# Kernel optimization log

Measured on AMD Instinct MI355X. Metric: run time of the kernel, lower is better.

## Reference

```python
import jax, jax.numpy as jnp
import numpy as np
from jax import lax

B, C_IN, H_IN, W_IN = 128, 256, 8, 32
RH, RW = 16, 64            # rec-head resolution
YOH, XOH = RH // 2, RW // 2  # onehot sizes (8, 32)
HID = 256
NC = 163                   # num classes == embed size
T = 32                     # target length
C_ENC = C_IN + XOH + YOH   # 296 encoder channels
L = (RH // 2) * (RW // 2)  # 256 attention positions


def setup_inputs() -> dict:
    key = jax.random.key(0)
    ks = jax.random.split(key, 18)
    s = 0.05
    return {
        "x": jax.random.normal(ks[0], (B, C_IN, H_IN, W_IN), jnp.float32),
        "decoder_targets": jax.random.randint(ks[1], (B, T), 0, NC),
        "word_targets": jax.random.randint(ks[2], (B, T), 0, NC),
        # seq_encoder conv 3x3
        "conv_w": jax.random.normal(ks[3], (C_IN, C_IN, 3, 3), jnp.float32) * 0.02,
        "conv_b": jnp.zeros((C_IN,), jnp.float32),
        # decoder embedding (post kaiming re-init => random, not identity)
        "emb_dec": jax.random.normal(ks[4], (NC, NC), jnp.float32) * s,
        "word_w": jax.random.normal(ks[5], (HID, NC), jnp.float32) * s,
        "word_b": jnp.zeros((HID,), jnp.float32),
        "attn_w": jax.random.normal(ks[6], (HID, 2 * HID + XOH + YOH), jnp.float32) * s,
        "attn_b": jnp.zeros((HID,), jnp.float32),
        "attn_v": jax.random.normal(ks[7], (HID,), jnp.float32) * (1.0 / np.sqrt(HID)),
        # GRUCell, gate order [r, z, n]
        "gru_wih": jax.random.normal(ks[8], (3 * HID, 2 * HID + XOH + YOH), jnp.float32) * s,
        "gru_bih": jnp.zeros((3 * HID,), jnp.float32),
        "gru_whh": jax.random.normal(ks[9], (3 * HID, HID), jnp.float32) * s,
        "gru_bhh": jnp.zeros((3 * HID,), jnp.float32),
        "out_w": jax.random.normal(ks[10], (NC, HID), jnp.float32) * s,
        "out_b": jnp.zeros((NC,), jnp.float32),
        # positional one-hot embedding tables (also kaiming re-initialized)
        "x_emb": jax.random.normal(ks[11], (XOH, XOH), jnp.float32) * s,
        "y_emb": jax.random.normal(ks[12], (YOH, YOH), jnp.float32) * s,
    }


def _forward(x, conv_w, conv_b, emb_dec, word_w, word_b, attn_w, attn_b, attn_v,
             gru_wih, gru_bih, gru_whh, gru_bhh, out_w, out_b, x_emb, y_emb,
             decoder_targets, word_targets):
    b = x.shape[0]
    # rescale: bilinear upsample (align_corners=False ~ half-pixel)
    xr = jax.image.resize(x, (b, C_IN, RH, RW), method="linear")
    # seq_encoder: conv3x3 + ReLU + maxpool2
    conv = lax.conv_general_dilated(xr, conv_w, (1, 1), "SAME",
                                    dimension_numbers=("NCHW", "OIHW", "NCHW"))
    conv = jax.nn.relu(conv + conv_b[None, :, None, None])
    pooled = lax.reduce_window(conv, -jnp.inf, lax.max,
                               (1, 1, 2, 2), (1, 1, 2, 2), "VALID")  # (B,256,8,32)
    hf, wf = RH // 2, RW // 2
    # positional channels: x_map[c,y,x] = x_emb[x,c]; y_map[c,y,x] = y_emb[y,c]
    x_map = jnp.broadcast_to(x_emb.T[:, None, :], (XOH, hf, wf))
    y_map = jnp.broadcast_to(y_emb.T[:, :, None], (YOH, hf, wf))
    x_map = jnp.broadcast_to(x_map[None], (b, XOH, hf, wf))
    y_map = jnp.broadcast_to(y_map[None], (b, YOH, hf, wf))
    feat = jnp.concatenate([pooled, x_map, y_map], axis=1)      # (B,296,8,32)
    enc = feat.reshape(b, C_ENC, hf * wf).transpose(0, 2, 1)    # (B, L, C)

    t_len = decoder_targets.shape[1]
    # teacher forcing: input at step 0 is BOS (=0), else previous target
    inputs_seq = jnp.concatenate(
        [jnp.zeros((b, 1), decoder_targets.dtype), decoder_targets[:, :-1]], axis=1)

    def step(hidden, xs):
        tok, tgt = xs
        we = emb_dec[tok] @ word_w.T + word_b                   # (B, HID)
        # Bahdanau attention
        hrep = jnp.broadcast_to(hidden[:, None, :], (b, enc.shape[1], HID))
        cat = jnp.concatenate([hrep, enc], axis=-1)             # (B,L,2H+OH)
        energy = jnp.tanh(jnp.einsum("blc,hc->blh", cat, attn_w) + attn_b)
        scores = jnp.einsum("blh,h->bl", energy, attn_v)
        w = jax.nn.softmax(scores, axis=1)                      # (B,L)
        ctx = jnp.einsum("bl,blc->bc", w, enc)                  # (B, C)
        rin = jnp.concatenate([we, ctx], axis=-1)               # (B, 2H+OH)
        # GRUCell
        gi = rin @ gru_wih.T + gru_bih
        gh = hidden @ gru_whh.T + gru_bhh
        i_r, i_z, i_n = jnp.split(gi, 3, axis=-1)
        h_r, h_z, h_n = jnp.split(gh, 3, axis=-1)
        r = jax.nn.sigmoid(i_r + h_r)
        z = jax.nn.sigmoid(i_z + h_z)
        n = jnp.tanh(i_n + r * h_n)
        h_new = (1.0 - z) * n + z * hidden
        logp = jax.nn.log_softmax(h_new @ out_w.T + out_b, axis=1)
        # NLLLoss(ignore_index=-1, reduction='none')
        nll = -jnp.take_along_axis(logp, jnp.clip(tgt, 0)[:, None], axis=1)[:, 0]
        nll = jnp.where(tgt >= 0, nll, 0.0)
        return h_new, nll

    h0 = jnp.zeros((b, HID), jnp.float32)
    _, nlls = lax.scan(step, h0, (inputs_seq.T, word_targets.T))  # (T, B)
    loss_vec = nlls.sum(axis=0)                                   # (B,)
    return 0.2 * (loss_vec.sum() / loss_vec.shape[0])


def reference(x, decoder_targets, word_targets, conv_w, conv_b, emb_dec,
              word_w, word_b, attn_w, attn_b, attn_v, gru_wih, gru_bih,
              gru_whh, gru_bhh, out_w, out_b, x_emb, y_emb):
    return _forward(x, conv_w, conv_b, emb_dec, word_w, word_b, attn_w, attn_b,
                    attn_v, gru_wih, gru_bih, gru_whh, gru_bhh, out_w, out_b,
                    x_emb, y_emb, decoder_targets, word_targets)
```

## Files before the change

### kernel.cpp

```cpp
#include <hip/hip_runtime.h>
#include <hip/hip_bf16.h>
#include <math.h>

#define B    128
#define CIN  256
#define HIN  8
#define WIN_ 32
#define RH   16
#define RW   64
#define HID  256
#define NC   163
#define T    32
#define L    256
#define CENC 296

typedef __attribute__((ext_vector_type(8))) short short8;
typedef __attribute__((ext_vector_type(8))) unsigned short u16x8;
typedef __attribute__((ext_vector_type(4))) float f32x4;

__device__ __forceinline__ float bf2f(unsigned short u) {
    unsigned int x = ((unsigned int)u) << 16;
    return __uint_as_float(x);
}
__device__ __forceinline__ unsigned short f2bf(float f) {
    unsigned int x = __float_as_uint(f);
    unsigned int r = (x + 0x7FFFu + ((x >> 16) & 1u)) >> 16;
    return (unsigned short)r;
}
__device__ __forceinline__ float fast_tanh(float x) {
    float e = __expf(2.f * x);
    return 1.f - 2.f * __builtin_amdgcn_rcpf(e + 1.f);
}
__device__ __forceinline__ float fast_sigm(float x) {
    return __builtin_amdgcn_rcpf(1.f + __expf(-x));
}
__device__ __forceinline__ float wave_red_max(float v) {
    #pragma unroll
    for (int o = 32; o > 0; o >>= 1) v = fmaxf(v, __shfl_down(v, o, 64));
    return v;
}
__device__ __forceinline__ float wave_red_sum(float v) {
    #pragma unroll
    for (int o = 32; o > 0; o >>= 1) v += __shfl_down(v, o, 64);
    return v;
}
__device__ __forceinline__ float half_red_sum(float v) {
    #pragma unroll
    for (int o = 16; o > 0; o >>= 1) v += __shfl_down(v, o, 64);
    return v;
}

__global__ void __launch_bounds__(256) k_upsxt(const float* __restrict__ x,
                                               unsigned short* __restrict__ Xt) {
    __shared__ __align__(16) float sf[64 * 2 * 32];
    const int y = blockIdx.x;
    const int b = blockIdx.y;
    const int tid = threadIdx.x;
    float sy = 0.5f * y - 0.25f;
    int yq0 = (y - 1) >> 1;
    float wy = sy - (float)yq0;
    int y0c = min(max(yq0, 0), HIN - 1);
    int y1c = min(max(yq0 + 1, 0), HIN - 1);
    const int xo = tid & 63;
    const int cj = tid >> 6;
    float sx = 0.5f * xo - 0.25f;
    int xq0 = (xo - 1) >> 1;
    float wx = sx - (float)xq0;
    int x0c = min(max(xq0, 0), WIN_ - 1);
    int x1c = min(max(xq0 + 1, 0), WIN_ - 1);
    for (int cc = 0; cc < 4; cc++) {
        __syncthreads();
        #pragma unroll
        for (int i = 0; i < 4; i++) {
            int idx = tid * 4 + i;
            int c = idx >> 4;
            int rowh = (idx >> 3) & 1;
            int part = idx & 7;
            int ysrc = rowh ? y1c : y0c;
            float4 v = *reinterpret_cast<const float4*>(
                x + ((size_t)(b * CIN + cc * 64 + c) * HIN + ysrc) * WIN_ + part * 4);
            *reinterpret_cast<float4*>(sf + ((c * 2 + rowh) * 32 + part * 4)) = v;
        }
        __syncthreads();
        unsigned short ov[16];
        #pragma unroll
        for (int j = 0; j < 16; j++) {
            int c = cj * 16 + j;
            const float* r0 = sf + (c * 2 + 0) * 32;
            const float* r1 = sf + (c * 2 + 1) * 32;
            float v = (1.f - wy) * ((1.f - wx) * r0[x0c] + wx * r0[x1c])
                    +        wy  * ((1.f - wx) * r1[x0c] + wx * r1[x1c]);
            ov[j] = f2bf(v);
        }
        unsigned short* dst = Xt + ((size_t)((b * 16 + y) * 64 + xo)) * 256 + cc * 64 + cj * 16;
        *reinterpret_cast<u16x8*>(dst)     = *reinterpret_cast<u16x8*>(ov);
        *reinterpret_cast<u16x8*>(dst + 8) = *reinterpret_cast<u16x8*>(ov + 8);
    }
}

__global__ void k_wt(const float* __restrict__ conv_w, unsigned short* __restrict__ Wt) {
    int e = blockIdx.x * 256 + threadIdx.x;
    int ci = e & 255;
    int co = (e >> 8) & 255;
    int s  = e >> 16;
    Wt[(size_t)(s * 256 + co) * 256 + ci] = f2bf(conv_w[(size_t)(co * 256 + ci) * 9 + s]);
}

__global__ void __launch_bounds__(256) k_convmm(const unsigned short* __restrict__ Xt,
        const unsigned short* __restrict__ Wt, const float* __restrict__ conv_b,
        unsigned short* __restrict__ enc_bf) {
    __shared__ __align__(16) char smem[36864];
    unsigned short* A_s = (unsigned short*)smem;
    unsigned short* B_s = A_s + 128 * 72;
    float* pool = (float*)smem;
    const int mt = blockIdx.x;
    const int n0 = blockIdx.y * 128;
    const int b = mt >> 3;
    const int y0 = (mt & 7) * 2;
    const int tid = threadIdx.x;
    const int wave = tid >> 6, lane = tid & 63;
    const int mq = (wave & 1) * 64, nq = (wave >> 1) * 64;
    const int lm = lane & 15, lq = lane >> 4;
    f32x4 acc[4][4];
    #pragma unroll
    for (int mi = 0; mi < 4; mi++)
        #pragma unroll
        for (int ni = 0; ni < 4; ni++)
            #pragma unroll
            for (int r = 0; r < 4; r++) acc[mi][ni][r] = 0.f;

    for (int s9 = 0; s9 < 9; s9++) {
        const int ky = s9 / 3, kx = s9 % 3;
        const unsigned short* Wb = Wt + (size_t)s9 * 256 * 256;
        for (int kc = 0; kc < 256; kc += 64) {
            __syncthreads();
            #pragma unroll
            for (int it = 0; it < 8; it++) {
                int s2 = tid + it * 256;
                int i = s2 & 1023;
                int row = i >> 3, q8 = i & 7;
                if (s2 < 1024) {
                    int yy = y0 + (row >> 6) + ky - 1;
                    int xx = (row & 63) + kx - 1;
                    u16x8 va = {0, 0, 0, 0, 0, 0, 0, 0};
                    if ((unsigned)yy < 16u && (unsigned)xx < 64u)
                        va = *reinterpret_cast<const u16x8*>(
                            Xt + ((size_t)((b * 16 + yy) * 64 + xx)) * 256 + kc + q8 * 8);
                    *reinterpret_cast<u16x8*>(A_s + row * 72 + q8 * 8) = va;
                } else {
                    u16x8 vb = *reinterpret_cast<const u16x8*>(
                        Wb + (size_t)(n0 + row) * 256 + kc + q8 * 8);
                    *reinterpret_cast<u16x8*>(B_s + row * 72 + q8 * 8) = vb;
                }
            }
            __syncthreads();
            for (int ks = 0; ks < 2; ks++) {
                short8 af[4], bfr[4];
                #pragma unroll
                for (int mi = 0; mi < 4; mi++)
                    af[mi] = *reinterpret_cast<const short8*>(
                        A_s + (mq + mi * 16 + lm) * 72 + ks * 32 + lq * 8);
                #pragma unroll
                for (int ni = 0; ni < 4; ni++)
                    bfr[ni] = *reinterpret_cast<const short8*>(
                        B_s + (nq + ni * 16 + lm) * 72 + ks * 32 + lq * 8);
                #pragma unroll
                for (int mi = 0; mi < 4; mi++)
                    #pragma unroll
                    for (int ni = 0; ni < 4; ni++)
                        acc[mi][ni] = __builtin_amdgcn_mfma_f32_16x16x32_bf16(
                            af[mi], bfr[ni], acc[mi][ni], 0, 0, 0);
            }
        }
    }
    __syncthreads();
    #pragma unroll
    for (int mi = 0; mi < 4; mi++) {
        int px0 = mi * 8 + lq * 2;
        #pragma unroll
        for (int ni = 0; ni < 4; ni++) {
            int nl = nq + ni * 16 + lm;
            float pa = fmaxf(acc[mi][ni][0], acc[mi][ni][1]);
            float pb = fmaxf(acc[mi][ni][2], acc[mi][ni][3]);
            pool[((wave & 1) * 32 + px0) * 132 + nl] = pa;
            pool[((wave & 1) * 32 + px0 + 1) * 132 + nl] = pb;
        }
    }
    __syncthreads();
    {
        int base = tid * 16;
        int px = base >> 7;
        int nb = base & 127;
        unsigned short ov[16];
        #pragma unroll
        for (int i = 0; i < 16; i++) {
            int n = nb + i;
            float v = fmaxf(pool[px * 132 + n], pool[(32 + px) * 132 + n]) + conv_b[n0 + n];
            ov[i] = f2bf(fmaxf(v, 0.f));
        }
        unsigned short* dst = enc_bf + ((size_t)b * L + (mt & 7) * 32 + px) * CENC + n0 + nb;
        *reinterpret_cast<u16x8*>(dst)     = *reinterpret_cast<u16x8*>(ov);
        *reinterpret_cast<u16x8*>(dst + 8) = *reinterpret_cast<u16x8*>(ov + 8);
    }
}

__global__ void k_encpos(const float* __restrict__ x_emb, const float* __restrict__ y_emb,
                         unsigned short* __restrict__ enc_bf, unsigned short* __restrict__ pos2t) {
    int b = blockIdx.x, l = threadIdx.x;
    int yl = l >> 5, xl = l & 31;
    unsigned short* e = enc_bf + (size_t)(b * L + l) * CENC + 256;
    #pragma unroll
    for (int c = 0; c < 32; c++) e[c] = f2bf(x_emb[xl * 32 + c]);
    #pragma unroll
    for (int c = 0; c < 8; c++) e[32 + c] = f2bf(y_emb[yl * 8 + c]);
    if (b == 0) {
        #pragma unroll
        for (int c = 0; c < 32; c++) pos2t[c * 256 + l] = f2bf(x_emb[xl * 32 + c]);
        #pragma unroll
        for (int c = 0; c < 8; c++) pos2t[(32 + c) * 256 + l] = f2bf(y_emb[yl * 8 + c]);
    }
}

__global__ void __launch_bounds__(256) k_enct(const unsigned short* __restrict__ enc_bf,
                                              unsigned short* __restrict__ enc_t) {
    __shared__ unsigned short s[64 * 264];
    const int c0 = blockIdx.x * 64;
    const int b = blockIdx.y;
    const int tid = threadIdx.x;
    #pragma unroll
    for (int j = 0; j < 8; j++) {
        u16x8 u = *reinterpret_cast<const u16x8*>(
            enc_bf + ((size_t)b * L + tid) * CENC + c0 + j * 8);
        #pragma unroll
        for (int k = 0; k < 8; k++) s[(j * 8 + k) * 264 + tid] = u[k];
    }
    __syncthreads();
    {
        int c = tid >> 2, lp = tid & 3;
        const unsigned short* row = s + c * 264 + lp * 64;
        unsigned short* dst = enc_t + ((size_t)b * 256 + c0 + c) * L + lp * 64;
        #pragma unroll
        for (int i = 0; i < 8; i++)
            *reinterpret_cast<u16x8*>(dst + i * 8) =
                *reinterpret_cast<const u16x8*>(row + i * 8);
    }
}

__global__ void __launch_bounds__(256) k_etab(const float* __restrict__ emb_dec,
                                              const float* __restrict__ word_w,
                                              const float* __restrict__ word_b,
                                              float* __restrict__ E) {
    __shared__ float er[NC];
    int row = blockIdx.x, tid = threadIdx.x;
    for (int k = tid; k < NC; k += 256) er[k] = emb_dec[(size_t)row * NC + k];
    __syncthreads();
    float a = word_b[tid];
    for (int k = 0; k < NC; k++) a += er[k] * word_w[(size_t)tid * NC + k];
    E[(size_t)row * HID + tid] = a;
}

__global__ void k_prep(const float* __restrict__ attn_w, const float* __restrict__ out_w,
                       unsigned short* __restrict__ wA_bf, unsigned short* __restrict__ ow_bf) {
    int o = blockIdx.x, k = threadIdx.x;
    wA_bf[(size_t)o * 256 + k] = f2bf(attn_w[(size_t)o * 552 + k]);
    if (o < NC) ow_bf[(size_t)o * 256 + k] = f2bf(out_w[(size_t)o * 256 + k]);
}

__global__ void __launch_bounds__(1024) k_wpack(const float* __restrict__ wih,
        const float* __restrict__ whh, unsigned short* __restrict__ WpackC,
        unsigned short* __restrict__ WpackH) {
    const int blk = blockIdx.x;
    const int tid = threadIdx.x;
    unsigned short o[8];
    if (blk < 37) {
        #pragma unroll
        for (int j = 0; j < 8; j++) {
            int k = blk * 8 + j;
            float v = (tid < 768) ? wih[(size_t)tid * 552 + 256 + k] : 0.f;
            o[j] = f2bf(v);
        }
        *reinterpret_cast<u16x8*>(WpackC + ((size_t)blk * 1024 + tid) * 8) =
            *reinterpret_cast<u16x8*>(o);
    } else {
        int it = blk - 37;
        #pragma unroll
        for (int j = 0; j < 8; j++) {
            int k = it * 8 + j;
            float v = (tid < 768) ? whh[(size_t)tid * 256 + k] : 0.f;
            o[j] = f2bf(v);
        }
        *reinterpret_cast<u16x8*>(WpackH + ((size_t)it * 1024 + tid) * 8) =
            *reinterpret_cast<u16x8*>(o);
    }
}

__global__ void __launch_bounds__(768) k_wge(const float* __restrict__ wih,
                                             unsigned short* __restrict__ WgE) {
    int k = blockIdx.x, g = threadIdx.x;
    WgE[(size_t)k * 768 + g] = f2bf(wih[(size_t)g * 552 + k]);
}
__global__ void __launch_bounds__(768) k_gie(const float* __restrict__ E,
                                             const unsigned short* __restrict__ WgE,
                                             const float* __restrict__ bih,
                                             float* __restrict__ giE) {
    __shared__ float er[256];
    int v = blockIdx.x, g = threadIdx.x;
    if (g < 256) er[g] = E[(size_t)v * 256 + g];
    __syncthreads();
    float a = bih[g];
    #pragma unroll 4
    for (int k = 0; k < 256; k++) a += er[k] * bf2f(WgE[(size_t)k * 768 + g]);
    giE[(size_t)v * 768 + g] = a;
}

__global__ void __launch_bounds__(256) k_ep(const unsigned short* __restrict__ enc_bf,
                                            const float* __restrict__ attn_w,
                                            unsigned short* __restrict__ ep_t) {
    __shared__ __align__(16) float eS[16][132];
    __shared__ __align__(16) float wS[16][36];
    const int l0 = blockIdx.x * 128;
    const int h0 = blockIdx.y * 32;
    const int b = blockIdx.z;
    const int tid = threadIdx.x;
    const int hh = tid >> 5, ll = tid & 31;
    float acc[4][4];
    #pragma unroll
    for (int s2 = 0; s2 < 4; s2++)
        #pragma unroll
        for (int r = 0; r < 4; r++) acc[s2][r] = 0.f;
    for (int kc = 0; kc < CENC; kc += 16) {
        const int kn = min(16, CENC - kc);
        __syncthreads();
        #pragma unroll
        for (int it = 0; it < 2; it++) {
            int idx = it * 256 + tid;
            int lq = idx >> 2, kq = idx & 3;
            float v0 = 0.f, v1 = 0.f, v2 = 0.f, v3 = 0.f;
            if (kq * 4 < kn) {
                ushort4 u = *reinterpret_cast<const ushort4*>(
                    enc_bf + (size_t)(b * L + l0 + lq) * CENC + kc + kq * 4);
                v0 = bf2f(u.x); v1 = bf2f(u.y); v2 = bf2f(u.z); v3 = bf2f(u.w);
            }
            eS[kq * 4 + 0][lq] = v0; eS[kq * 4 + 1][lq] = v1;
            eS[kq * 4 + 2][lq] = v2; eS[kq * 4 + 3][lq] = v3;
        }
        if (tid < 128) {
            int hq = tid >> 2, kq = tid & 3;
            float4 v = make_float4(0.f, 0.f, 0.f, 0.f);
            if (kq * 4 < kn)
                v = *reinterpret_cast<const float4*>(attn_w + (size_t)(h0 + hq) * 552 + 256 + kc + kq * 4);
            wS[kq * 4 + 0][hq] = v.x; wS[kq * 4 + 1][hq] = v.y;
            wS[kq * 4 + 2][hq] = v.z; wS[kq * 4 + 3][hq] = v.w;
        }
        __syncthreads();
        #pragma unroll
        for (int k = 0; k < 16; k++) {
            float4 e = *reinterpret_cast<const float4*>(&eS[k][ll * 4]);
            float4 w = *reinterpret_cast<const float4*>(&wS[k][hh * 4]);
            float ev[4] = {e.x, e.y, e.z, e.w};
            float wv[4] = {w.x, w.y, w.z, w.w};
            #pragma unroll
            for (int s2 = 0; s2 < 4; s2++)
                #pragma unroll
                for (int r = 0; r < 4; r++) acc[s2][r] += wv[s2] * ev[r];
        }
    }
    #pragma unroll
    for (int r = 0; r < 4; r++) {
        ushort4 o;
        o.x = f2bf(acc[0][r]); o.y = f2bf(acc[1][r]);
        o.z = f2bf(acc[2][r]); o.w = f2bf(acc[3][r]);
        *reinterpret_cast<ushort4*>(
            ep_t + ((size_t)(b * L) + l0 + ll * 4 + r) * HID + h0 + hh * 4) = o;
    }
}

__global__ void k_init(int* __restrict__ flagH, int* __restrict__ flagS) {
    if (threadIdx.x < B) { flagH[threadIdx.x] = 0; flagS[threadIdx.x] = 0; }
}

__global__ void __launch_bounds__(1024) k_steps(
        const float* __restrict__ giE, const float* __restrict__ bhh,
        const unsigned short* __restrict__ ep_t, const unsigned short* __restrict__ enc_t,
        const unsigned short* __restrict__ wA_bf, const unsigned short* __restrict__ ow_bf,
        const unsigned short* __restrict__ pos2t,
        const unsigned short* __restrict__ WpackC, const unsigned short* __restrict__ WpackH,
        const float* __restrict__ attn_b, const float* __restrict__ attn_v,
        const float* __restrict__ out_b,
        const int* __restrict__ dec_tgt, const int* __restrict__ word_tgt,
        float* __restrict__ nllG,
        unsigned int* __restrict__ hX32, unsigned int* __restrict__ sX32,
        int* __restrict__ flagH, int* __restrict__ flagS) {
    const int bid = blockIdx.x;
    const bool roleA = bid < B;
    const int b = bid & (B - 1);
    const int tid = threadIdx.x;
    const int hwid = tid >> 5, l32 = tid & 31;

    __shared__ __align__(16) unsigned short big[L * 256];
    __shared__ __align__(16) unsigned short hmail[256];
    __shared__ __align__(16) unsigned short swl[256];
    __shared__ __align__(16) float rinF[552];
    __shared__ __align__(16) float hF[256];
    __shared__ __align__(16) float hpF[256], vbF[256], swlF[256];
    __shared__ float hfS[256];
    __shared__ float scr[256];
    __shared__ float red[16];
    __shared__ float rzS[512], inS[256], hnS[256];
    unsigned int* hmail32 = reinterpret_cast<unsigned int*>(hmail);
    unsigned int* swl32 = reinterpret_cast<unsigned int*>(swl);

    if (roleA) {
        if (tid < 256) vbF[tid] = attn_v[tid];
        {
            const u16x8* src = reinterpret_cast<const u16x8*>(ep_t + (size_t)b * L * 256);
            u16x8* dst = reinterpret_cast<u16x8*>(big);
            #pragma unroll
            for (int i = 0; i < 8; i++) dst[tid + i * 1024] = src[tid + i * 1024];
        }
        float nllacc = 0.f;
        __syncthreads();
        for (int t = 0; t <= T; t++) {
            if (tid == 0) {
                while (__hip_atomic_load(&flagH[b], __ATOMIC_RELAXED,
                                         __HIP_MEMORY_SCOPE_AGENT) < t + 1)
                    __builtin_amdgcn_s_sleep(1);
            }
            __syncthreads();
            if (tid < 128) {
                unsigned int u = __hip_atomic_load(&hX32[b * 128 + tid], __ATOMIC_RELAXED,
                                                   __HIP_MEMORY_SCOPE_AGENT);
                hF[2 * tid]     = bf2f((unsigned short)(u & 0xffffu));
                hF[2 * tid + 1] = bf2f((unsigned short)(u >> 16));
            }
            __syncthreads();
            if (t < T) {
                #pragma unroll
                for (int it = 0; it < 8; it++) {
                    int row = it * 32 + hwid;
                    u16x8 w = *reinterpret_cast<const u16x8*>(wA_bf + (size_t)row * 256 + l32 * 8);
                    float4 ha = *reinterpret_cast<const float4*>(hF + l32 * 8);
                    float4 hb = *reinterpret_cast<const float4*>(hF + l32 * 8 + 4);
                    float d = bf2f(w[0]) * ha.x + bf2f(w[1]) * ha.y
                            + bf2f(w[2]) * ha.z + bf2f(w[3]) * ha.w
                            + bf2f(w[4]) * hb.x + bf2f(w[5]) * hb.y
                            + bf2f(w[6]) * hb.z + bf2f(w[7]) * hb.w;
                    d = half_red_sum(d);
                    if (l32 == 0) hpF[row] = d + attn_b[row];
                }
                __syncthreads();
                #pragma unroll
                for (int it = 0; it < 8; it++) {
                    int row = it * 32 + hwid;
                    u16x8 e = *reinterpret_cast<const u16x8*>(big + (size_t)row * 256 + l32 * 8);
                    float4 ha = *reinterpret_cast<const float4*>(hpF + l32 * 8);
                    float4 hb = *reinterpret_cast<const float4*>(hpF + l32 * 8 + 4);
                    float4 va = *reinterpret_cast<const float4*>(vbF + l32 * 8);
                    float4 vv = *reinterpret_cast<const float4*>(vbF + l32 * 8 + 4);
                    float d = va.x * fast_tanh(bf2f(e[0]) + ha.x)
                            + va.y * fast_tanh(bf2f(e[1]) + ha.y)
                            + va.z * fast_tanh(bf2f(e[2]) + ha.z)
                            + va.w * fast_tanh(bf2f(e[3]) + ha.w)
                            + vv.x * fast_tanh(bf2f(e[4]) + hb.x)
                            + vv.y * fast_tanh(bf2f(e[5]) + hb.y)
                            + vv.z * fast_tanh(bf2f(e[6]) + hb.z)
                            + vv.w * fast_tanh(bf2f(e[7]) + hb.w);
                    d = half_red_sum(d);
                    if (l32 == 0) scr[row] = d;
                }
                __syncthreads();
                float sc = -1e30f;
                if (tid < 256) {
                    sc = scr[tid];
                    float m = wave_red_max(sc);
                    if ((tid & 63) == 0) red[tid >> 6] = m;
                }
                __syncthreads();
                float M2 = fmaxf(fmaxf(red[0], red[1]), fmaxf(red[2], red[3]));
                float e2 = 0.f;
                if (tid < 256) {
                    e2 = __expf(sc - M2);
                    float sm = wave_red_sum(e2);
                    if ((tid & 63) == 0) red[8 + (tid >> 6)] = sm;
                }
                __syncthreads();
                if (tid < 256) {
                    float invS = __builtin_amdgcn_rcpf(red[8] + red[9] + red[10] + red[11]);
                    swl[tid] = f2bf(e2 * invS);
                }
                __syncthreads();
                if (tid < 128)
                    __hip_atomic_store(&sX32[b * 128 + tid], swl32[tid], __ATOMIC_RELAXED,
                                       __HIP_MEMORY_SCOPE_AGENT);
                __syncthreads();
                if (tid == 0)
                    __hip_atomic_store(&flagS[b], t + 1, __ATOMIC_RELAXED,
                                       __HIP_MEMORY_SCOPE_AGENT);
            }
            if (t > 0) {
                #pragma unroll
                for (int it = 0; it < 6; it++) {
                    int row = it * 32 + hwid;
                    float d = 0.f;
                    if (row < NC) {
                        u16x8 w = *reinterpret_cast<const u16x8*>(ow_bf + (size_t)row * 256 + l32 * 8);
                        float4 ha = *reinterpret_cast<const float4*>(hF + l32 * 8);
                        float4 hb = *reinterpret_cast<const float4*>(hF + l32 * 8 + 4);
                        d = bf2f(w[0]) * ha.x + bf2f(w[1]) * ha.y
                          + bf2f(w[2]) * ha.z + bf2f(w[3]) * ha.w
                          + bf2f(w[4]) * hb.x + bf2f(w[5]) * hb.y
                          + bf2f(w[6]) * hb.z + bf2f(w[7]) * hb.w;
                    }
                    d = half_red_sum(d);
                    if (l32 == 0 && row < NC) scr[row] = d + out_b[row];
                }
                __syncthreads();
                float lg = -1e30f;
                if (tid < 256) {
                    if (tid < NC) lg = scr[tid];
                    float m = wave_red_max(lg);
                    if ((tid & 63) == 0) red[tid >> 6] = m;
                }
                __syncthreads();
                float M = fmaxf(fmaxf(red[0], red[1]), fmaxf(red[2], red[3]));
                if (tid < 256) {
                    float e = (tid < NC) ? __expf(lg - M) : 0.f;
                    float sm = wave_red_sum(e);
                    if ((tid & 63) == 0) red[8 + (tid >> 6)] = sm;
                }
                __syncthreads();
                if (tid == 0) {
                    float S = red[8] + red[9] + red[10] + red[11];
                    int tgt = word_tgt[b * T + (t - 1)];
                    if (tgt >= 0) nllacc += M + __logf(S) - scr[tgt];
                }
                __syncthreads();
            }
        }
        if (tid == 0) nllG[b] = nllacc;
    } else {
        {
            const u16x8* src = reinterpret_cast<const u16x8*>(enc_t + (size_t)b * 256 * 256);
            u16x8* dst = reinterpret_cast<u16x8*>(big);
            #pragma unroll
            for (int i = 0; i < 8; i++) dst[tid + i * 1024] = src[tid + i * 1024];
        }
        __syncthreads();
        for (int t = 0; t <= T; t++) {
            if (tid < 256) {
                float h;
                if (t == 0) {
                    h = 0.f;
                } else {
                    float hold = hfS[tid];
                    int tokp = (t == 1) ? 0 : dec_tgt[b * T + (t - 2)];
                    const float* gE = giE + (size_t)tokp * 768;
                    float r_ = fast_sigm(rzS[tid] + gE[tid] + bhh[tid]);
                    float z_ = fast_sigm(rzS[256 + tid] + gE[256 + tid] + bhh[256 + tid]);
                    float n_ = fast_tanh(inS[tid] + gE[512 + tid] + r_ * (hnS[tid] + bhh[512 + tid]));
                    h = (1.f - z_) * n_ + z_ * hold;
                }
                hfS[tid] = h;
                hmail[tid] = f2bf(h);
                rinF[296 + tid] = h;
            }
            __syncthreads();
            if (tid < 128)
                __hip_atomic_store(&hX32[b * 128 + tid], hmail32[tid], __ATOMIC_RELAXED,
                                   __HIP_MEMORY_SCOPE_AGENT);
            __syncthreads();
            if (tid == 0)
                __hip_atomic_store(&flagH[b], t + 1, __ATOMIC_RELAXED,
                                   __HIP_MEMORY_SCOPE_AGENT);
            if (t == T) break;
            float hacc = 0.f;
            if (tid < 768) {
                float a0 = 0.f, a1 = 0.f;
                #pragma unroll 4
                for (int it = 0; it < 32; it++) {
                    u16x8 w = *reinterpret_cast<const u16x8*>(WpackH + ((size_t)it * 1024 + tid) * 8);
                    float4 ra = *reinterpret_cast<const float4*>(rinF + 296 + it * 8);
                    float4 rb = *reinterpret_cast<const float4*>(rinF + 296 + it * 8 + 4);
                    a0 += bf2f(w[0]) * ra.x + bf2f(w[2]) * ra.z
                        + bf2f(w[4]) * rb.x + bf2f(w[6]) * rb.z;
                    a1 += bf2f(w[1]) * ra.y + bf2f(w[3]) * ra.w
                        + bf2f(w[5]) * rb.y + bf2f(w[7]) * rb.w;
                }
                hacc = a0 + a1;
            }
            if (tid == 0) {
                while (__hip_atomic_load(&flagS[b], __ATOMIC_RELAXED,
                                         __HIP_MEMORY_SCOPE_AGENT) < t + 1)
                    __builtin_amdgcn_s_sleep(1);
            }
            __syncthreads();
            if (tid < 128) {
                unsigned int u = __hip_atomic_load(&sX32[b * 128 + tid], __ATOMIC_RELAXED,
                                                   __HIP_MEMORY_SCOPE_AGENT);
                swlF[2 * tid]     = bf2f((unsigned short)(u & 0xffffu));
                swlF[2 * tid + 1] = bf2f((unsigned short)(u >> 16));
            }
            __syncthreads();
            #pragma unroll
            for (int it = 0; it < 8; it++) {
                int row = it * 32 + hwid;
                u16x8 e = *reinterpret_cast<const u16x8*>(big + (size_t)row * 256 + l32 * 8);
                float4 sa = *reinterpret_cast<const float4*>(swlF + l32 * 8);
                float4 sb = *reinterpret_cast<const float4*>(swlF + l32 * 8 + 4);
                float d = bf2f(e[0]) * sa.x + bf2f(e[1]) * sa.y
                        + bf2f(e[2]) * sa.z + bf2f(e[3]) * sa.w
                        + bf2f(e[4]) * sb.x + bf2f(e[5]) * sb.y
                        + bf2f(e[6]) * sb.z + bf2f(e[7]) * sb.w;
                d = half_red_sum(d);
                if (l32 == 0) rinF[row] = d;
            }
            #pragma unroll
            for (int it = 0; it < 2; it++) {
                int row = it * 32 + hwid;
                float d = 0.f;
                if (row < 40) {
                    u16x8 p = *reinterpret_cast<const u16x8*>(pos2t + (size_t)row * 256 + l32 * 8);
                    float4 sa = *reinterpret_cast<const float4*>(swlF + l32 * 8);
                    float4 sb = *reinterpret_cast<const float4*>(swlF + l32 * 8 + 4);
                    d = bf2f(p[0]) * sa.x + bf2f(p[1]) * sa.y
                      + bf2f(p[2]) * sa.z + bf2f(p[3]) * sa.w
                      + bf2f(p[4]) * sb.x + bf2f(p[5]) * sb.y
                      + bf2f(p[6]) * sb.z + bf2f(p[7]) * sb.w;
                }
                d = half_red_sum(d);
                if (l32 == 0 && row < 40) rinF[256 + row] = d;
            }
            __syncthreads();
            if (tid < 768) {
                float c0 = 0.f, c1 = 0.f;
                #pragma unroll 4
                for (int it = 0; it < 37; it++) {
                    u16x8 w = *reinterpret_cast<const u16x8*>(WpackC + ((size_t)it * 1024 + tid) * 8);
                    float4 ra = *reinterpret_cast<const float4*>(rinF + it * 8);
                    float4 rb = *reinterpret_cast<const float4*>(rinF + it * 8 + 4);
                    c0 += bf2f(w[0]) * ra.x + bf2f(w[2]) * ra.z
                        + bf2f(w[4]) * rb.x + bf2f(w[6]) * rb.z;
                    c1 += bf2f(w[1]) * ra.y + bf2f(w[3]) * ra.w
                        + bf2f(w[5]) * rb.y + bf2f(w[7]) * rb.w;
                }
                float cacc = c0 + c1;
                if (tid < 512) rzS[tid] = cacc + hacc;
                else { inS[tid - 512] = cacc; hnS[tid - 512] = hacc; }
            }
            __syncthreads();
        }
    }
}

__global__ void k_reduce(const float* __restrict__ nll, float* __restrict__ out) {
    __shared__ float red[2];
    float v = nll[threadIdx.x];
    v = wave_red_sum(v);
    if ((threadIdx.x & 63) == 0) red[threadIdx.x >> 6] = v;
    __syncthreads();
    if (threadIdx.x == 0) out[0] = 0.2f * (red[0] + red[1]) * (1.f / 128.f);
}

extern "C" void kernel_launch(void* const* d_in, const int* in_sizes, int n_in,
                              void* d_out, int out_size, void* d_ws, size_t ws_size,
                              hipStream_t stream) {
    const float* x        = (const float*)d_in[0];
    const int*   dec_tgt  = (const int*)d_in[1];
    const int*   word_tgt = (const int*)d_in[2];
    const float* conv_w   = (const float*)d_in[3];
    const float* conv_b   = (const float*)d_in[4];
    const float* emb_dec  = (const float*)d_in[5];
    const float* word_w   = (const float*)d_in[6];
    const float* word_b   = (const float*)d_in[7];
    const float* attn_w   = (const float*)d_in[8];
    const float* attn_b   = (const float*)d_in[9];
    const float* attn_v   = (const float*)d_in[10];
    const float* gru_wih  = (const float*)d_in[11];
    const float* gru_bih  = (const float*)d_in[12];
    const float* gru_whh  = (const float*)d_in[13];
    const float* gru_bhh  = (const float*)d_in[14];
    const float* out_w    = (const float*)d_in[15];
    const float* out_b    = (const float*)d_in[16];
    const float* x_emb    = (const float*)d_in[17];
    const float* y_emb    = (const float*)d_in[18];

    char* ws = (char*)d_ws;
    size_t off = 0;
    auto alloc = [&](size_t bytes) -> void* {
        void* p = ws + off;
        off = (off + bytes + 255) & ~(size_t)255;
        return p;
    };
    unsigned short* Xt     = (unsigned short*)alloc((size_t)B * 16 * 64 * 256 * 2);
    unsigned short* enc_bf = (unsigned short*)alloc((size_t)B * L * CENC * 2);
    unsigned short* Wt     = (unsigned short*)alloc((size_t)9 * 256 * 256 * 2);
    float* E      = (float*)alloc((size_t)NC * HID * 4);
    unsigned short* wA_bf  = (unsigned short*)alloc((size_t)HID * HID * 2);
    unsigned short* ow_bf  = (unsigned short*)alloc((size_t)NC * HID * 2);
    unsigned short* WpackC = (unsigned short*)alloc((size_t)37 * 1024 * 8 * 2);
    unsigned short* WpackH = (unsigned short*)alloc((size_t)32 * 1024 * 8 * 2);
    unsigned short* WgE    = (unsigned short*)alloc((size_t)256 * 768 * 2);
    float* giE    = (float*)alloc((size_t)NC * 768 * 4);
    unsigned short* pos2t  = (unsigned short*)alloc((size_t)40 * 256 * 2);
    float* nllG   = (float*)alloc((size_t)B * 4);
    unsigned int* hX32     = (unsigned int*)alloc((size_t)B * 128 * 4);
    unsigned int* sX32     = (unsigned int*)alloc((size_t)B * 128 * 4);
    int* flagH    = (int*)alloc((size_t)B * 4);
    int* flagS    = (int*)alloc((size_t)B * 4);
    unsigned short* ep_t  = Xt;
    unsigned short* enc_t = Xt + (size_t)B * L * HID;
    float* out    = (float*)d_out;

    hipLaunchKernelGGL(k_init, dim3(1), dim3(256), 0, stream, flagH, flagS);
    hipLaunchKernelGGL(k_upsxt, dim3(16, 128), dim3(256), 0, stream, x, Xt);
    hipLaunchKernelGGL(k_wt, dim3(2304), dim3(256), 0, stream, conv_w, Wt);
    hipLaunchKernelGGL(k_encpos, dim3(128), dim3(256), 0, stream, x_emb, y_emb, enc_bf, pos2t);
    hipLaunchKernelGGL(k_convmm, dim3(1024, 2), dim3(256), 0, stream, Xt, Wt, conv_b, enc_bf);
    hipLaunchKernelGGL(k_etab, dim3(163), dim3(256), 0, stream, emb_dec, word_w, word_b, E);
    hipLaunchKernelGGL(k_prep, dim3(256), dim3(256), 0, stream, attn_w, out_w, wA_bf, ow_bf);
    hipLaunchKernelGGL(k_wpack, dim3(69), dim3(1024), 0, stream, gru_wih, gru_whh, WpackC, WpackH);
    hipLaunchKernelGGL(k_wge, dim3(256), dim3(768), 0, stream, gru_wih, WgE);
    hipLaunchKernelGGL(k_gie, dim3(163), dim3(768), 0, stream, E, WgE, gru_bih, giE);
    hipLaunchKernelGGL(k_ep, dim3(2, 8, 128), dim3(256), 0, stream, enc_bf, attn_w, ep_t);
    hipLaunchKernelGGL(k_enct, dim3(4, 128), dim3(256), 0, stream, enc_bf, enc_t);
    hipLaunchKernelGGL(k_steps, dim3(256), dim3(1024), 0, stream,
                       giE, gru_bhh, ep_t, enc_t, wA_bf, ow_bf, pos2t, WpackC, WpackH,
                       attn_b, attn_v, out_b, dec_tgt, word_tgt, nllG,
                       hX32, sX32, flagH, flagS);
    hipLaunchKernelGGL(k_reduce, dim3(1), dim3(128), 0, stream, nllG, out);
}
```

Baseline: 1.253 ms.

## Pad shared vectors against bank conflicts, shrink conv K-chunk, spin-wait in all readers

The conv GEMM's K-chunk per stage drops from 64 to 32 with a row pitch of 40, shrinking shared memory and simplifying the staging loads. In the recurrent kernel the hidden, attention and word vectors in shared memory are padded (8 of every 12 floats used) so the per-lane float4 reads avoid bank conflicts. The flag spin-wait now runs in all 128 reader threads instead of thread 0 followed by a barrier, removing one __syncthreads per handshake. In exchange the conv loop has twice as many barriers per K, and many threads now poll global flags at once.

```diff
diff --git a/kernel.cpp b/kernel.cpp
--- a/kernel.cpp
+++ b/kernel.cpp
@@ -17,6 +17,8 @@
 typedef __attribute__((ext_vector_type(8))) short short8;
 typedef __attribute__((ext_vector_type(8))) unsigned short u16x8;
 typedef __attribute__((ext_vector_type(4))) float f32x4;
+
+#define PH(k) ((((k) >> 3) * 12) + ((k) & 7))
 
 __device__ __forceinline__ float bf2f(unsigned short u) {
     unsigned int x = ((unsigned int)u) << 16;
@@ -109,9 +111,9 @@
 __global__ void __launch_bounds__(256) k_convmm(const unsigned short* __restrict__ Xt,
         const unsigned short* __restrict__ Wt, const float* __restrict__ conv_b,
         unsigned short* __restrict__ enc_bf) {
-    __shared__ __align__(16) char smem[36864];
+    __shared__ __align__(16) char smem[34048];
     unsigned short* A_s = (unsigned short*)smem;
-    unsigned short* B_s = A_s + 128 * 72;
+    unsigned short* B_s = A_s + 128 * 40;
     float* pool = (float*)smem;
     const int mt = blockIdx.x;
     const int n0 = blockIdx.y * 128;
@@ -132,45 +134,37 @@
     for (int s9 = 0; s9 < 9; s9++) {
         const int ky = s9 / 3, kx = s9 % 3;
         const unsigned short* Wb = Wt + (size_t)s9 * 256 * 256;
-        for (int kc = 0; kc < 256; kc += 64) {
+        for (int kc = 0; kc < 256; kc += 32) {
             __syncthreads();
             #pragma unroll
-            for (int it = 0; it < 8; it++) {
+            for (int it = 0; it < 2; it++) {
                 int s2 = tid + it * 256;
-                int i = s2 & 1023;
-                int row = i >> 3, q8 = i & 7;
-                if (s2 < 1024) {
-                    int yy = y0 + (row >> 6) + ky - 1;
-                    int xx = (row & 63) + kx - 1;
-                    u16x8 va = {0, 0, 0, 0, 0, 0, 0, 0};
-                    if ((unsigned)yy < 16u && (unsigned)xx < 64u)
-                        va = *reinterpret_cast<const u16x8*>(
-                            Xt + ((size_t)((b * 16 + yy) * 64 + xx)) * 256 + kc + q8 * 8);
-                    *reinterpret_cast<u16x8*>(A_s + row * 72 + q8 * 8) = va;
-                } else {
-                    u16x8 vb = *reinterpret_cast<const u16x8*>(
-                        Wb + (size_t)(n0 + row) * 256 + kc + q8 * 8);
-                    *reinterpret_cast<u16x8*>(B_s + row * 72 + q8 * 8) = vb;
-                }
+                int pix = s2 >> 2, q4 = s2 & 3;
+                int yy = y0 + (pix >> 6) + ky - 1;
+                int xx = (pix & 63) + kx - 1;
+                u16x8 va = {0, 0, 0, 0, 0, 0, 0, 0};
+                if ((unsigned)yy < 16u && (unsigned)xx < 64u)
+                    va = *reinterpret_cast<const u16x8*>(
+                        Xt + ((size_t)((b * 16 + yy) * 64 + xx)) * 256 + kc + q4 * 8);
+                *reinterpret_cast<u16x8*>(A_s + pix * 40 + q4 * 8) = va;
+                u16x8 vb = *reinterpret_cast<const u16x8*>(
+                    Wb + (size_t)(n0 + pix) * 256 + kc + q4 * 8);
+                *reinterpret_cast<u16x8*>(B_s + pix * 40 + q4 * 8) = vb;
             }
             __syncthreads();
-            for (int ks = 0; ks < 2; ks++) {
-                short8 af[4], bfr[4];
-                #pragma unroll
-                for (int mi = 0; mi < 4; mi++)
-                    af[mi] = *reinterpret_cast<const short8*>(
-                        A_s + (mq + mi * 16 + lm) * 72 + ks * 32 + lq * 8);
+            short8 af[4], bfr[4];
+            #pragma unroll
+            for (int mi = 0; mi < 4; mi++)
+                af[mi] = *reinterpret_cast<const short8*>(A_s + (mq + mi * 16 + lm) * 40 + lq * 8);
+            #pragma unroll
+            for (int ni = 0; ni < 4; ni++)
+                bfr[ni] = *reinterpret_cast<const short8*>(B_s + (nq + ni * 16 + lm) * 40 + lq * 8);
+            #pragma unroll
+            for (int mi = 0; mi < 4; mi++)
                 #pragma unroll
                 for (int ni = 0; ni < 4; ni++)
-                    bfr[ni] = *reinterpret_cast<const short8*>(
-                        B_s + (nq + ni * 16 + lm) * 72 + ks * 32 + lq * 8);
-                #pragma unroll
-                for (int mi = 0; mi < 4; mi++)
-                    #pragma unroll
-                    for (int ni = 0; ni < 4; ni++)
-                        acc[mi][ni] = __builtin_amdgcn_mfma_f32_16x16x32_bf16(
-                            af[mi], bfr[ni], acc[mi][ni], 0, 0, 0);
-            }
+                    acc[mi][ni] = __builtin_amdgcn_mfma_f32_16x16x32_bf16(
+                        af[mi], bfr[ni], acc[mi][ni], 0, 0, 0);
         }
     }
     __syncthreads();
@@ -401,8 +395,8 @@
     __shared__ __align__(16) unsigned short hmail[256];
     __shared__ __align__(16) unsigned short swl[256];
     __shared__ __align__(16) float rinF[552];
-    __shared__ __align__(16) float hF[256];
-    __shared__ __align__(16) float hpF[256], vbF[256], swlF[256];
+    __shared__ __align__(16) float hF[384];
+    __shared__ __align__(16) float hpF[384], vbF[384], swlF[384];
     __shared__ float hfS[256];
     __shared__ float scr[256];
     __shared__ float red[16];
@@ -411,7 +405,7 @@
     unsigned int* swl32 = reinterpret_cast<unsigned int*>(swl);
 
     if (roleA) {
-        if (tid < 256) vbF[tid] = attn_v[tid];
+        if (tid < 256) vbF[PH(tid)] = attn_v[tid];
         {
             const u16x8* src = reinterpret_cast<const u16x8*>(ep_t + (size_t)b * L * 256);
             u16x8* dst = reinterpret_cast<u16x8*>(big);
@@ -421,17 +415,14 @@
         float nllacc = 0.f;
         __syncthreads();
         for (int t = 0; t <= T; t++) {
-            if (tid == 0) {
+            if (tid < 128) {
                 while (__hip_atomic_load(&flagH[b], __ATOMIC_RELAXED,
                                          __HIP_MEMORY_SCOPE_AGENT) < t + 1)
                     __builtin_amdgcn_s_sleep(1);
-            }
-            __syncthreads();
-            if (tid < 128) {
                 unsigned int u = __hip_atomic_load(&hX32[b * 128 + tid], __ATOMIC_RELAXED,
                                                    __HIP_MEMORY_SCOPE_AGENT);
-                hF[2 * tid]     = bf2f((unsigned short)(u & 0xffffu));
-                hF[2 * tid + 1] = bf2f((unsigned short)(u >> 16));
+                hF[PH(2 * tid)]     = bf2f((unsigned short)(u & 0xffffu));
+                hF[PH(2 * tid + 1)] = bf2f((unsigned short)(u >> 16));
             }
             __syncthreads();
             if (t < T) {
@@ -439,24 +430,24 @@
                 for (int it = 0; it < 8; it++) {
                     int row = it * 32 + hwid;
                     u16x8 w = *reinterpret_cast<const u16x8*>(wA_bf + (size_t)row * 256 + l32 * 8);
-                    float4 ha = *reinterpret_cast<const float4*>(hF + l32 * 8);
-                    float4 hb = *reinterpret_cast<const float4*>(hF + l32 * 8 + 4);
+                    float4 ha = *reinterpret_cast<const float4*>(hF + l32 * 12);
+                    float4 hb = *reinterpret_cast<const float4*>(hF + l32 * 12 + 4);
                     float d = bf2f(w[0]) * ha.x + bf2f(w[1]) * ha.y
                             + bf2f(w[2]) * ha.z + bf2f(w[3]) * ha.w
                             + bf2f(w[4]) * hb.x + bf2f(w[5]) * hb.y
                             + bf2f(w[6]) * hb.z + bf2f(w[7]) * hb.w;
                     d = half_red_sum(d);
-                    if (l32 == 0) hpF[row] = d + attn_b[row];
+                    if (l32 == 0) hpF[PH(row)] = d + attn_b[row];
                 }
                 __syncthreads();
                 #pragma unroll
                 for (int it = 0; it < 8; it++) {
                     int row = it * 32 + hwid;
                     u16x8 e = *reinterpret_cast<const u16x8*>(big + (size_t)row * 256 + l32 * 8);
-                    float4 ha = *reinterpret_cast<const float4*>(hpF + l32 * 8);
-                    float4 hb = *reinterpret_cast<const float4*>(hpF + l32 * 8 + 4);
-                    float4 va = *reinterpret_cast<const float4*>(vbF + l32 * 8);
-                    float4 vv = *reinterpret_cast<const float4*>(vbF + l32 * 8 + 4);
+                    float4 ha = *reinterpret_cast<const float4*>(hpF + l32 * 12);
+                    float4 hb = *reinterpret_cast<const float4*>(hpF + l32 * 12 + 4);
+                    float4 va = *reinterpret_cast<const float4*>(vbF + l32 * 12);
+                    float4 vv = *reinterpret_cast<const float4*>(vbF + l32 * 12 + 4);
                     float d = va.x * fast_tanh(bf2f(e[0]) + ha.x)
                             + va.y * fast_tanh(bf2f(e[1]) + ha.y)
                             + va.z * fast_tanh(bf2f(e[2]) + ha.z)
@@ -504,8 +495,8 @@
                     float d = 0.f;
                     if (row < NC) {
                         u16x8 w = *reinterpret_cast<const u16x8*>(ow_bf + (size_t)row * 256 + l32 * 8);
-                        float4 ha = *reinterpret_cast<const float4*>(hF + l32 * 8);
-                        float4 hb = *reinterpret_cast<const float4*>(hF + l32 * 8 + 4);
+                        float4 ha = *reinterpret_cast<const float4*>(hF + l32 * 12);
+                        float4 hb = *reinterpret_cast<const float4*>(hF + l32 * 12 + 4);
                         d = bf2f(w[0]) * ha.x + bf2f(w[1]) * ha.y
                           + bf2f(w[2]) * ha.z + bf2f(w[3]) * ha.w
                           + bf2f(w[4]) * hb.x + bf2f(w[5]) * hb.y
@@ -588,25 +579,22 @@
                 }
                 hacc = a0 + a1;
             }
-            if (tid == 0) {
+            if (tid < 128) {
                 while (__hip_atomic_load(&flagS[b], __ATOMIC_RELAXED,
                                          __HIP_MEMORY_SCOPE_AGENT) < t + 1)
                     __builtin_amdgcn_s_sleep(1);
-            }
-            __syncthreads();
-            if (tid < 128) {
                 unsigned int u = __hip_atomic_load(&sX32[b * 128 + tid], __ATOMIC_RELAXED,
                                                    __HIP_MEMORY_SCOPE_AGENT);
-                swlF[2 * tid]     = bf2f((unsigned short)(u & 0xffffu));
-                swlF[2 * tid + 1] = bf2f((unsigned short)(u >> 16));
+                swlF[PH(2 * tid)]     = bf2f((unsigned short)(u & 0xffffu));
+                swlF[PH(2 * tid + 1)] = bf2f((unsigned short)(u >> 16));
             }
             __syncthreads();
             #pragma unroll
             for (int it = 0; it < 8; it++) {
                 int row = it * 32 + hwid;
                 u16x8 e = *reinterpret_cast<const u16x8*>(big + (size_t)row * 256 + l32 * 8);
-                float4 sa = *reinterpret_cast<const float4*>(swlF + l32 * 8);
-                float4 sb = *reinterpret_cast<const float4*>(swlF + l32 * 8 + 4);
+                float4 sa = *reinterpret_cast<const float4*>(swlF + l32 * 12);
+                float4 sb = *reinterpret_cast<const float4*>(swlF + l32 * 12 + 4);
                 float d = bf2f(e[0]) * sa.x + bf2f(e[1]) * sa.y
                         + bf2f(e[2]) * sa.z + bf2f(e[3]) * sa.w
                         + bf2f(e[4]) * sb.x + bf2f(e[5]) * sb.y
@@ -620,8 +608,8 @@
                 float d = 0.f;
                 if (row < 40) {
                     u16x8 p = *reinterpret_cast<const u16x8*>(pos2t + (size_t)row * 256 + l32 * 8);
-                    float4 sa = *reinterpret_cast<const float4*>(swlF + l32 * 8);
-                    float4 sb = *reinterpret_cast<const float4*>(swlF + l32 * 8 + 4);
+                    float4 sa = *reinterpret_cast<const float4*>(swlF + l32 * 12);
+                    float4 sb = *reinterpret_cast<const float4*>(swlF + l32 * 12 + 4);
                     d = bf2f(p[0]) * sa.x + bf2f(p[1]) * sa.y
                       + bf2f(p[2]) * sa.z + bf2f(p[3]) * sa.w
                       + bf2f(p[4]) * sb.x + bf2f(p[5]) * sb.y
```

Result: faster. 1.182 ms (-5.7%).
